# Kernel tuning notes

Measured on AMD Instinct MI355X. Metric: run time of the kernel, lower is better.

## Reference

```python
import jax, jax.numpy as jnp
import numpy as np

EPS = 1e-5
NUM_GROUPS = 32


def setup_inputs() -> dict:
    key = jax.random.key(0)
    ks = jax.random.split(key, 4)
    B, C, H, W = 8, 128, 64, 64
    x = jax.random.normal(ks[0], (B, C, H, W), dtype=jnp.float32)
    gamma = jnp.ones((C,), dtype=jnp.float32)
    beta = jnp.zeros((C,), dtype=jnp.float32)
    # 1x1 convs stored as dense [out, in] matrices (kaiming-ish scale)
    w_qkv = jax.random.normal(ks[1], (3 * C, C), dtype=jnp.float32) * (1.0 / np.sqrt(C))
    b_qkv = jnp.zeros((3 * C,), dtype=jnp.float32)
    w_out = jax.random.normal(ks[2], (C, C), dtype=jnp.float32) * (1.0 / np.sqrt(C))
    b_out = jnp.zeros((C,), dtype=jnp.float32)
    return {"x": x, "gamma": gamma, "beta": beta, "w_qkv": w_qkv,
            "b_qkv": b_qkv, "w_out": w_out, "b_out": b_out}


def _group_norm(x, gamma, beta):
    B, C, H, W = x.shape
    xg = x.reshape(B, NUM_GROUPS, C // NUM_GROUPS, H, W)
    mean = jnp.mean(xg, axis=(2, 3, 4), keepdims=True)
    var = jnp.var(xg, axis=(2, 3, 4), keepdims=True)
    xn = ((xg - mean) * jax.lax.rsqrt(var + EPS)).reshape(B, C, H, W)
    return xn * gamma[None, :, None, None] + beta[None, :, None, None]


def reference(x, gamma, beta, w_qkv, b_qkv, w_out, b_out):
    B, C, H, W = x.shape
    hw = H * W
    xn = _group_norm(x, gamma, beta)
    # 1x1 conv C -> 3C
    qkv = jnp.einsum('oc,bchw->bohw', w_qkv, xn) + b_qkv[None, :, None, None]
    q, k, v = jnp.split(qkv, 3, axis=1)           # each [B, C, H, W]
    q = q.reshape(B, C, hw).transpose(0, 2, 1)    # [B, hw, C]
    k = k.reshape(B, C, hw)                       # [B, C, hw]
    v = v.reshape(B, C, hw).transpose(0, 2, 1)    # [B, hw, C]
    scale = C ** (-0.5)
    weights = jnp.einsum('bnc,bcm->bnm', q, k) * scale  # [B, hw, hw]
    attn = jax.nn.softmax(weights, axis=-1)
    out = jnp.einsum('bnm,bmc->bnc', attn, v)     # [B, hw, C]
    out = out.reshape(B, H, W, C).transpose(0, 3, 1, 2)  # [B, C, H, W]
    out = jnp.einsum('oc,bchw->bohw', w_out, out) + b_out[None, :, None, None]
    return out + x
```

## Files before the change

kernel.cpp:

```cpp
#include <hip/hip_runtime.h>

typedef __attribute__((ext_vector_type(8))) short short8;
typedef __attribute__((ext_vector_type(4))) float f32x4;
typedef unsigned short u16;
typedef unsigned int u32;

__device__ __forceinline__ float bf2f(u16 h) {
  union { u32 u; float f; } c; c.u = ((u32)h) << 16; return c.f;
}
__device__ __forceinline__ u16 f2bf(float f) {
  union { float f; u32 u; } c; c.f = f;
  u32 u = c.u;
  u32 r = u + 0x7fffu + ((u >> 16) & 1u);
  return (u16)(r >> 16);
}
__device__ __forceinline__ f32x4 mfma16(short8 a, short8 b, f32x4 c) {
  return __builtin_amdgcn_mfma_f32_16x16x32_bf16(a, b, c, 0, 0, 0);
}
__device__ __forceinline__ u32 cvtpk(float lo, float hi) {
  u32 r;
  asm("v_cvt_pk_bf16_f32 %0, %1, %2" : "=v"(r) : "v"(lo), "v"(hi));
  return r;
}
__device__ __forceinline__ void gl2lds(const u16* g, u16* l) {
  __builtin_amdgcn_global_load_lds(
      (const __attribute__((address_space(1))) void*)g,
      (__attribute__((address_space(3))) void*)l, 16, 0, 0);
}

#define WAIT_BAR(N) \
  asm volatile("s_waitcnt vmcnt(" #N ")\n\ts_barrier" ::: "memory")
#define MEM_FENCE() asm volatile("" ::: "memory")

__device__ __forceinline__ bool bf_mode(const void* gamma) {
  return ((const u16*)gamma)[0] == 0x3F80u;
}
__device__ __forceinline__ void load8(const void* p, size_t idx, bool isbf,
                                      float* o) {
  if (isbf) {
    const u16* q = (const u16*)p + idx;
    uint4 v = *(const uint4*)q;
    u32 w[4] = {v.x, v.y, v.z, v.w};
#pragma unroll
    for (int j = 0; j < 4; ++j) {
      o[2 * j]     = bf2f((u16)(w[j] & 0xffffu));
      o[2 * j + 1] = bf2f((u16)(w[j] >> 16));
    }
  } else {
    const float* q = (const float*)p + idx;
    float4 a = *(const float4*)q;
    float4 b = *(const float4*)(q + 4);
    o[0] = a.x; o[1] = a.y; o[2] = a.z; o[3] = a.w;
    o[4] = b.x; o[5] = b.y; o[6] = b.z; o[7] = b.w;
  }
}
__device__ __forceinline__ float ldf(const void* p, size_t i, bool isbf) {
  return isbf ? bf2f(((const u16*)p)[i]) : ((const float*)p)[i];
}

__global__ __launch_bounds__(256) void stats_kernel(
    const void* __restrict__ x, const void* __restrict__ gamma,
    const void* __restrict__ w_qkv, const void* __restrict__ w_out,
    u16* __restrict__ w_bf, float* __restrict__ stats) {
  bool isbf = bf_mode(gamma);
  int bg = blockIdx.x;
  if (!isbf) {
    int i = bg * 256 + threadIdx.x;
    float v = (i < 49152) ? ((const float*)w_qkv)[i]
                          : ((const float*)w_out)[i - 49152];
    w_bf[i] = f2bf(v);
  }
  int b = bg >> 5, g = bg & 31;
  size_t base = ((size_t)b * 128 + g * 4) << 12;
  float s = 0.f, ss = 0.f;
  for (int i = threadIdx.x; i < 2048; i += 256) {
    float v[8];
    load8(x, base + (size_t)i * 8, isbf, v);
#pragma unroll
    for (int j = 0; j < 8; ++j) { s += v[j]; ss += v[j] * v[j]; }
  }
#pragma unroll
  for (int off = 32; off; off >>= 1) {
    s += __shfl_xor(s, off);
    ss += __shfl_xor(ss, off);
  }
  __shared__ float red[8];
  int wv = threadIdx.x >> 6, lane = threadIdx.x & 63;
  if (lane == 0) { red[wv] = s; red[4 + wv] = ss; }
  __syncthreads();
  if (threadIdx.x == 0) {
    float st = red[0] + red[1] + red[2] + red[3];
    float sst = red[4] + red[5] + red[6] + red[7];
    float mean = st * (1.f / 16384.f);
    float var = sst * (1.f / 16384.f) - mean * mean;
    stats[bg * 2] = mean;
    stats[bg * 2 + 1] = rsqrtf(var + 1e-5f);
  }
}

__global__ __launch_bounds__(256) void qkv_fused_kernel(
    const void* __restrict__ x, const float* __restrict__ stats,
    const void* __restrict__ gamma, const void* __restrict__ beta,
    const void* __restrict__ w_qkv_in, const void* __restrict__ b_qkv,
    const u16* __restrict__ w_bf, u16* __restrict__ Qt,
    u16* __restrict__ Kt_bfm, u16* __restrict__ Kt_fpm,
    u16* __restrict__ V) {
  bool isbf = bf_mode(gamma);
  const u16* wq = isbf ? (const u16*)w_qkv_in : w_bf;
  u16* Kt = isbf ? Kt_bfm : Kt_fpm;
  int nt = blockIdx.x, b = blockIdx.y;
  int n0 = nt * 64;
  int t = threadIdx.x;
  __shared__ __align__(16) u16 shb[9216];
  u16* xn = shb;
  {
    int cg = t >> 3, ng = t & 7;
    float mean = stats[(b * 32 + cg) * 2];
    float rstd = stats[(b * 32 + cg) * 2 + 1];
    float vals[4][8];
#pragma unroll
    for (int cc = 0; cc < 4; ++cc) {
      int c = cg * 4 + cc;
      float sc = ldf(gamma, c, isbf) * rstd;
      float sh = ldf(beta, c, isbf) - mean * sc;
      float v[8];
      load8(x, (((size_t)b * 128 + c) << 12) + n0 + ng * 8, isbf, v);
#pragma unroll
      for (int j = 0; j < 8; ++j) vals[cc][j] = v[j] * sc + sh;
    }
#pragma unroll
    for (int j = 0; j < 8; ++j) {
      ushort4 o;
      o.x = f2bf(vals[0][j]);
      o.y = f2bf(vals[1][j]);
      o.z = f2bf(vals[2][j]);
      o.w = f2bf(vals[3][j]);
      *(ushort4*)(xn + (ng * 8 + j) * 136 + cg * 4) = o;
    }
  }
  __syncthreads();
  int wv = t >> 6, lane = t & 63, l15 = lane & 15, quad = lane >> 4;
  short8 bfr[4][4];
#pragma unroll
  for (int mt = 0; mt < 4; ++mt)
#pragma unroll
    for (int kk = 0; kk < 4; ++kk)
      bfr[mt][kk] = *(const short8*)(xn + (mt * 16 + l15) * 136 + kk * 32 + quad * 8);
  __syncthreads();

  u16* res = shb;
#pragma unroll
  for (int g = 0; g < 3; ++g) {
#pragma unroll
    for (int rd = 0; rd < 2; ++rd) {
      int tl = rd * 4 + wv;
      int otg = g * 8 + tl;
      short8 a[4];
#pragma unroll
      for (int kk = 0; kk < 4; ++kk)
        a[kk] = *(const short8*)(wq + (size_t)(otg * 16 + l15) * 128 + kk * 32 + quad * 8);
      int o0 = otg * 16 + quad * 4;
      float bias[4];
#pragma unroll
      for (int r = 0; r < 4; ++r) bias[r] = ldf(b_qkv, o0 + r, isbf);
      int c0 = tl * 16 + quad * 4;
#pragma unroll
      for (int mt = 0; mt < 4; ++mt) {
        f32x4 acc = (f32x4){0.f, 0.f, 0.f, 0.f};
#pragma unroll
        for (int kk = 0; kk < 4; ++kk) acc = mfma16(a[kk], bfr[mt][kk], acc);
        int nl = mt * 16 + l15;
        if (g < 2) {
          ushort4 o;
          o.x = f2bf(acc[0] + bias[0]);
          o.y = f2bf(acc[1] + bias[1]);
          o.z = f2bf(acc[2] + bias[2]);
          o.w = f2bf(acc[3] + bias[3]);
          *(ushort4*)(res + nl * 136 + c0) = o;
        } else {
#pragma unroll
          for (int r = 0; r < 4; ++r)
            res[(c0 + r) * 72 + nl] = f2bf(acc[r] + bias[r]);
        }
      }
    }
    __syncthreads();
    if (g < 2) {
      int n = t >> 2, seg = t & 3;
      const uint4* src = (const uint4*)(res + n * 136 + seg * 32);
      uint4* dst = (uint4*)((g == 0 ? Qt : Kt) +
                            ((size_t)b * 4096 + n0 + n) * 128 + seg * 32);
#pragma unroll
      for (int i = 0; i < 4; ++i) dst[i] = src[i];
    } else {
      int c = t >> 1, hf = t & 1;
      const uint4* src = (const uint4*)(res + c * 72 + hf * 32);
      uint4* dst = (uint4*)(V + ((size_t)b * 128 + c) * 4096 + n0 + hf * 32);
#pragma unroll
      for (int i = 0; i < 4; ++i) dst[i] = src[i];
    }
    __syncthreads();
  }
}

__global__ __launch_bounds__(512, 1) void flash_kernel(
    const u16* __restrict__ Qt, const u16* __restrict__ Kt_bfm,
    const u16* __restrict__ Kt_fpm, const u16* __restrict__ V,
    u16* __restrict__ attn, const void* __restrict__ gamma, int fuse,
    const void* __restrict__ w_out_in, const u16* __restrict__ w_bf_out,
    const void* __restrict__ b_out, const void* __restrict__ x,
    void* __restrict__ out) {
  bool isbf = bf_mode(gamma);
  const u16* Kt = isbf ? Kt_bfm : Kt_fpm;
  int b = blockIdx.x, qt = blockIdx.y;
  int t = threadIdx.x;
  int wv = t >> 6, lane = t & 63;
  int l15 = lane & 15, quad = lane >> 4;
  int rset = wv >> 1, h = wv & 1;
  __shared__ __align__(16) u16 smem[32768];
  u16* kb0 = smem;
  u16* vb0 = smem + 16384;
  const u16* Kb = Kt + (size_t)b * 4096 * 128;
  const u16* Vg = V + (size_t)b * 128 * 4096;

  auto issueK = [&](int tile, u16* dst) {
    int m = tile * 64;
#pragma unroll
    for (int i2 = 0; i2 < 2; ++i2) {
      int i = wv * 2 + i2;
      int Rp = i * 4 + (lane >> 4);
      int Rs = (Rp & 32) | ((Rp & 12) << 1) | ((Rp & 16) >> 2) | (Rp & 3);
      gl2lds(Kb + (size_t)(m + Rs) * 128 + (((lane & 15) ^ (Rp & 15)) << 3),
             dst + i * 512);
    }
  };
  auto issueV = [&](int tile, u16* dst) {
    int m = tile * 64;
#pragma unroll
    for (int i2 = 0; i2 < 2; ++i2) {
      int i = wv * 2 + i2;
      int c = i * 8 + (lane >> 3);
      gl2lds(Vg + (size_t)c * 4096 + m + (((lane & 7) ^ (c & 7)) << 3),
             dst + i * 512);
    }
  };

  int wq = qt * 128 + rset * 32;
  const float qs = 0.12753251f;
  const float M = 10.0f;
  short8 qf[2][4];
#pragma unroll
  for (int rs = 0; rs < 2; ++rs)
#pragma unroll
    for (int kk = 0; kk < 4; ++kk) {
      short8 raw = *(const short8*)(
          Qt + ((size_t)b * 4096 + wq + rs * 16 + l15) * 128 + kk * 32 + quad * 8);
      short8 o;
#pragma unroll
      for (int j = 0; j < 8; ++j) o[j] = (short)f2bf(bf2f((u16)raw[j]) * qs);
      qf[rs][kk] = o;
    }
  asm volatile("s_waitcnt vmcnt(0)" ::: "memory");

  issueK(0, kb0);
  MEM_FENCE();
  issueV(0, vb0);
  MEM_FENCE();
  issueK(1, kb0 + 8192);
  MEM_FENCE();

  float ls[2] = {0.f, 0.f};
  f32x4 acc[2][8];
#pragma unroll
  for (int rs = 0; rs < 2; ++rs)
#pragma unroll
    for (int ct = 0; ct < 8; ++ct) acc[rs][ct] = (f32x4){0.f, 0.f, 0.f, 0.f};

  for (int kt = 0; kt < 64; ++kt) {
    int s = kt & 1;
    u16* kbs = kb0 + s * 8192;
    u16* vbs = vb0 + s * 8192;
    if (kt < 63) { WAIT_BAR(4); } else { WAIT_BAR(2); }
    if (kt < 63) issueV(kt + 1, vb0 + (s ^ 1) * 8192);
    MEM_FENCE();
    f32x4 sacc[2][2];
#pragma unroll
    for (int rs = 0; rs < 2; ++rs)
#pragma unroll
      for (int mt = 0; mt < 2; ++mt) sacc[rs][mt] = (f32x4){0.f, 0.f, 0.f, 0.f};
    __builtin_amdgcn_s_setprio(1);
#pragma unroll
    for (int mt = 0; mt < 2; ++mt) {
      int R = h * 32 + mt * 16 + l15;
      short8 kf[4];
#pragma unroll
      for (int kk = 0; kk < 4; ++kk)
        kf[kk] = *(const short8*)(&kbs[R * 128 + (((kk * 4 + quad) ^ l15) << 3)]);
#pragma unroll
      for (int rs = 0; rs < 2; ++rs)
#pragma unroll
        for (int kk = 0; kk < 4; ++kk)
          sacc[rs][mt] = mfma16(kf[kk], qf[rs][kk], sacc[rs][mt]);
    }
    __builtin_amdgcn_s_setprio(0);
    short8 pa[2];
#pragma unroll
    for (int rs = 0; rs < 2; ++rs) {
      union { u32 w[4]; short8 s8; } pk;
#pragma unroll
      for (int mt = 0; mt < 2; ++mt)
#pragma unroll
        for (int pr = 0; pr < 2; ++pr) {
          float p0 = __builtin_amdgcn_exp2f(sacc[rs][mt][2 * pr] - M);
          float p1 = __builtin_amdgcn_exp2f(sacc[rs][mt][2 * pr + 1] - M);
          ls[rs] += p0 + p1;
          pk.w[mt * 2 + pr] = cvtpk(p0, p1);
        }
      pa[rs] = pk.s8;
    }
    if (kt < 63) { WAIT_BAR(4); } else { WAIT_BAR(0); }
    if (kt < 62) issueK(kt + 2, kbs);
    MEM_FENCE();
    __builtin_amdgcn_s_setprio(1);
#pragma unroll
    for (int ct = 0; ct < 8; ++ct) {
      int c = ct * 16 + l15;
      int ch = ((h * 4 + quad) ^ (c & 7)) & 7;
      short8 vbf = *(const short8*)(&vbs[c * 64 + ch * 8]);
      acc[0][ct] = mfma16(pa[0], vbf, acc[0][ct]);
      acc[1][ct] = mfma16(pa[1], vbf, acc[1][ct]);
    }
    __builtin_amdgcn_s_setprio(0);
  }
  __syncthreads();

  float lsum[2][4];
#pragma unroll
  for (int rs = 0; rs < 2; ++rs) {
    float v = ls[rs];
    v += __shfl_xor(v, 16);
    v += __shfl_xor(v, 32);
#pragma unroll
    for (int r = 0; r < 4; ++r)
      lsum[rs][r] = __shfl(v, quad * 20 + r);
  }

  if (!fuse) {
    float* ef = (float*)smem;
#pragma unroll
    for (int rs = 0; rs < 2; ++rs) {
      if (h) {
#pragma unroll
        for (int ct = 0; ct < 8; ++ct)
          *(f32x4*)&ef[((rset * 8 + ct) * 64 + lane) * 4] = acc[rs][ct];
        if (rs == 0) {
#pragma unroll
          for (int j = 0; j < 8; ++j)
            ef[8192 + (rset * 64 + lane) * 8 + j] = lsum[j >> 2][j & 3];
        }
      }
      __syncthreads();
      if (!h) {
#pragma unroll
        for (int ct = 0; ct < 8; ++ct) {
          f32x4 o = *(const f32x4*)&ef[((rset * 8 + ct) * 64 + lane) * 4];
          acc[rs][ct] += o;
        }
        if (rs == 0) {
#pragma unroll
          for (int j = 0; j < 8; ++j)
            lsum[j >> 2][j & 3] += ef[8192 + (rset * 64 + lane) * 8 + j];
        }
      }
      __syncthreads();
    }
    if (!h) {
#pragma unroll
      for (int rs = 0; rs < 2; ++rs)
#pragma unroll
        for (int r = 0; r < 4; ++r) lsum[rs][r] = 1.f / lsum[rs][r];
#pragma unroll
      for (int rs = 0; rs < 2; ++rs)
#pragma unroll
        for (int ct = 0; ct < 8; ++ct)
#pragma unroll
          for (int r = 0; r < 4; ++r) {
            int n = wq + rs * 16 + quad * 4 + r;
            attn[((size_t)b * 4096 + n) * 128 + ct * 16 + l15] =
                f2bf(acc[rs][ct][r] * lsum[rs][r]);
          }
    }
    return;
  }

  const u16* wo = isbf ? (const u16*)w_out_in : w_bf_out;
  int o_row = wv * 16;
  int o0 = o_row + quad * 4;
  int nbase = qt * 128;
  float xres[8][4];
#pragma unroll
  for (int nt16 = 0; nt16 < 8; ++nt16)
#pragma unroll
    for (int r = 0; r < 4; ++r) {
      size_t idx = ((size_t)b * 128 + o0 + r) * 4096 + nbase + nt16 * 16 + l15;
      xres[nt16][r] = ldf(x, idx, isbf);
    }
  short8 wa[4];
#pragma unroll
  for (int kk = 0; kk < 4; ++kk)
    wa[kk] = *(const short8*)(wo + (size_t)(o_row + l15) * 128 + kk * 32 + quad * 8);

  u16* Otile = smem;
  float* mrg = (float*)(smem + 17408);
  float* lmr = (float*)(smem + 25600);
  if (h) {
#pragma unroll
    for (int j = 0; j < 8; ++j)
      lmr[(rset * 64 + lane) * 8 + j] = lsum[j >> 2][j & 3];
  }
  __syncthreads();
  if (!h) {
#pragma unroll
    for (int rs = 0; rs < 2; ++rs)
#pragma unroll
      for (int r = 0; r < 4; ++r)
        lsum[rs][r] =
            1.f / (lsum[rs][r] + lmr[(rset * 64 + lane) * 8 + rs * 4 + r]);
  }
  __syncthreads();
#pragma unroll
  for (int rs = 0; rs < 2; ++rs)
#pragma unroll
    for (int cg2 = 0; cg2 < 2; ++cg2) {
      if (h) {
#pragma unroll
        for (int c4 = 0; c4 < 4; ++c4)
          *(f32x4*)&mrg[((rset * 4 + c4) * 64 + lane) * 4] = acc[rs][cg2 * 4 + c4];
      }
      __syncthreads();
      if (!h) {
#pragma unroll
        for (int c4 = 0; c4 < 4; ++c4) {
          int ct = cg2 * 4 + c4;
          f32x4 o = *(const f32x4*)&mrg[((rset * 4 + c4) * 64 + lane) * 4];
          int nloc = rset * 32 + rs * 16 + quad * 4;
#pragma unroll
          for (int r = 0; r < 4; ++r)
            Otile[(nloc + r) * 136 + ct * 16 + l15] =
                f2bf((acc[rs][ct][r] + o[r]) * lsum[rs][r]);
        }
      }
      __syncthreads();
    }
  f32x4 acc2[8];
#pragma unroll
  for (int nt16 = 0; nt16 < 8; ++nt16) {
    acc2[nt16] = (f32x4){0.f, 0.f, 0.f, 0.f};
#pragma unroll
    for (int kk = 0; kk < 4; ++kk) {
      short8 bfrag = *(const short8*)(
          &Otile[(nt16 * 16 + l15) * 136 + kk * 32 + quad * 8]);
      acc2[nt16] = mfma16(wa[kk], bfrag, acc2[nt16]);
    }
  }
  float bias[4];
#pragma unroll
  for (int r = 0; r < 4; ++r) bias[r] = ldf(b_out, o0 + r, isbf);
#pragma unroll
  for (int nt16 = 0; nt16 < 8; ++nt16) {
#pragma unroll
    for (int r = 0; r < 4; ++r) {
      size_t idx = ((size_t)b * 128 + o0 + r) * 4096 + nbase + nt16 * 16 + l15;
      float val = acc2[nt16][r] + bias[r] + xres[nt16][r];
      if (isbf) ((u16*)out)[idx] = f2bf(val);
      else      ((float*)out)[idx] = val;
    }
  }
}

__global__ __launch_bounds__(256) void proj_kernel(
    const u16* __restrict__ attn, const void* __restrict__ w_out_in,
    const u16* __restrict__ w_bf_out, const void* __restrict__ b_out,
    const void* __restrict__ x, const void* __restrict__ gamma,
    void* __restrict__ out) {
  bool isbf = bf_mode(gamma);
  const u16* wo = isbf ? (const u16*)w_out_in : w_bf_out;
  int nt = blockIdx.x, ot = blockIdx.y, b = blockIdx.z;
  int wv = threadIdx.x >> 6, lane = threadIdx.x & 63;
  int l15 = lane & 15, quad = lane >> 4;
  int o_row = ot * 64 + wv * 16;
  short8 a[4];
#pragma unroll
  for (int kk = 0; kk < 4; ++kk)
    a[kk] = *(const short8*)(wo + (size_t)(o_row + l15) * 128 + kk * 32 + quad * 8);
  const u16* bbase = attn + ((size_t)b * 4096 + nt * 64) * 128;
  f32x4 acc[4];
#pragma unroll
  for (int mt = 0; mt < 4; ++mt) {
    acc[mt] = (f32x4){0.f, 0.f, 0.f, 0.f};
#pragma unroll
    for (int kk = 0; kk < 4; ++kk) {
      short8 bf = *(const short8*)(bbase + (size_t)(mt * 16 + l15) * 128 + kk * 32 + quad * 8);
      acc[mt] = mfma16(a[kk], bf, acc[mt]);
    }
  }
  int o0 = o_row + quad * 4;
  float bias[4];
#pragma unroll
  for (int r = 0; r < 4; ++r) bias[r] = ldf(b_out, o0 + r, isbf);
#pragma unroll
  for (int mt = 0; mt < 4; ++mt) {
    int n = nt * 64 + mt * 16 + l15;
#pragma unroll
    for (int r = 0; r < 4; ++r) {
      size_t idx = ((size_t)b * 128 + o0 + r) * 4096 + n;
      float val = acc[mt][r] + bias[r] + ldf(x, idx, isbf);
      if (isbf) ((u16*)out)[idx] = f2bf(val);
      else      ((float*)out)[idx] = val;
    }
  }
}

__global__ __launch_bounds__(256) void copy_kernel(
    const void* __restrict__ x, const void* __restrict__ gamma,
    void* __restrict__ out, int n) {
  bool isbf = bf_mode(gamma);
  int i = blockIdx.x * 256 + threadIdx.x;
  if (i < n) {
    if (isbf) ((u16*)out)[i] = ((const u16*)x)[i];
    else      ((float*)out)[i] = ((const float*)x)[i];
  }
}

extern "C" void kernel_launch(void* const* d_in, const int* in_sizes, int n_in,
                              void* d_out, int out_size, void* d_ws, size_t ws_size,
                              hipStream_t stream) {
  (void)in_sizes; (void)n_in;
  const void* x     = d_in[0];
  const void* gamma = d_in[1];
  const void* beta  = d_in[2];
  const void* w_qkv = d_in[3];
  const void* b_qkv = d_in[4];
  const void* w_out = d_in[5];
  const void* b_out = d_in[6];
  char* ws = (char*)d_ws;

  const size_t MB = 1u << 20;
  const size_t need = 16 * MB + 4096;
  if (ws_size < need) {
    copy_kernel<<<dim3((out_size + 255) / 256), dim3(256), 0, stream>>>(
        x, gamma, d_out, out_size);
    return;
  }
  int fuse = (ws_size >= 24 * MB + 262144) ? 1 : 0;
  u16 *Qt, *Kt_bfm, *Kt_fpm, *Vb, *w_bf, *attn;
  float* stats;
  if (fuse) {
    Qt     = (u16*)ws;
    Kt_bfm = (u16*)(ws + 8 * MB);
    Kt_fpm = Kt_bfm;
    Vb     = (u16*)(ws + 16 * MB);
    stats  = (float*)(ws + 24 * MB);
    w_bf   = (u16*)(ws + 24 * MB + 4096);
    attn   = Qt;
  } else {
    Qt     = (u16*)ws;
    Kt_bfm = (u16*)(ws + 8 * MB);
    w_bf   = (u16*)(ws + 8 * MB + 4096);
    stats  = (float*)(ws + 16 * MB);
    Vb     = (u16*)d_out;
    Kt_fpm = (u16*)d_out + 4194304;
    attn   = Qt;
  }

  stats_kernel<<<dim3(256), dim3(256), 0, stream>>>(
      x, gamma, w_qkv, w_out, w_bf, stats);
  qkv_fused_kernel<<<dim3(64, 8), dim3(256), 0, stream>>>(
      x, stats, gamma, beta, w_qkv, b_qkv, w_bf, Qt, Kt_bfm, Kt_fpm, Vb);
  flash_kernel<<<dim3(8, 32), dim3(512), 0, stream>>>(
      Qt, Kt_bfm, Kt_fpm, Vb, attn, gamma, fuse,
      w_out, w_bf + 49152, b_out, x, d_out);
  if (!fuse)
    proj_kernel<<<dim3(64, 2, 8), dim3(256), 0, stream>>>(
        attn, w_out, w_bf + 49152, b_out, x, gamma, d_out);
}
```

Measured before the change: 178.7 us.

## Restructure flash K/V prefetch into single-barrier double buffer with precomputed pointers

Replaces the staggered K/V prefetch schedule (K two tiles ahead, V one tile ahead, two waits and barriers per iteration) with a simpler double buffer. It issues K and V for the next tile together after a single full wait and barrier. Global source pointers are computed once and advanced by a fixed stride instead of recomputing the swizzled addresses each time. The loop is unrolled by two so the buffer index is a constant. This removes one barrier per iteration and some address arithmetic, but the prefetch distance for K drops from two tiles to one and each wait drains all outstanding loads, which may expose more memory latency.

```diff
diff --git a/kernel.cpp b/kernel.cpp
--- a/kernel.cpp
+++ b/kernel.cpp
@@ -218,32 +218,21 @@
   int l15 = lane & 15, quad = lane >> 4;
   int rset = wv >> 1, h = wv & 1;
   __shared__ __align__(16) u16 smem[32768];
-  u16* kb0 = smem;
-  u16* vb0 = smem + 16384;
   const u16* Kb = Kt + (size_t)b * 4096 * 128;
   const u16* Vg = V + (size_t)b * 128 * 4096;
 
-  auto issueK = [&](int tile, u16* dst) {
-    int m = tile * 64;
-#pragma unroll
-    for (int i2 = 0; i2 < 2; ++i2) {
-      int i = wv * 2 + i2;
-      int Rp = i * 4 + (lane >> 4);
-      int Rs = (Rp & 32) | ((Rp & 12) << 1) | ((Rp & 16) >> 2) | (Rp & 3);
-      gl2lds(Kb + (size_t)(m + Rs) * 128 + (((lane & 15) ^ (Rp & 15)) << 3),
-             dst + i * 512);
-    }
-  };
-  auto issueV = [&](int tile, u16* dst) {
-    int m = tile * 64;
-#pragma unroll
-    for (int i2 = 0; i2 < 2; ++i2) {
-      int i = wv * 2 + i2;
-      int c = i * 8 + (lane >> 3);
-      gl2lds(Vg + (size_t)c * 4096 + m + (((lane & 7) ^ (c & 7)) << 3),
-             dst + i * 512);
-    }
-  };
+  const u16 *kp0, *kp1, *vp0, *vp1;
+  {
+    int i0 = wv * 2, i1 = wv * 2 + 1;
+    int Rp0 = i0 * 4 + (lane >> 4), Rp1 = i1 * 4 + (lane >> 4);
+    int Rs0 = (Rp0 & 32) | ((Rp0 & 12) << 1) | ((Rp0 & 16) >> 2) | (Rp0 & 3);
+    int Rs1 = (Rp1 & 32) | ((Rp1 & 12) << 1) | ((Rp1 & 16) >> 2) | (Rp1 & 3);
+    kp0 = Kb + (size_t)Rs0 * 128 + (((lane & 15) ^ (Rp0 & 15)) << 3);
+    kp1 = Kb + (size_t)Rs1 * 128 + (((lane & 15) ^ (Rp1 & 15)) << 3);
+    int c0 = i0 * 8 + (lane >> 3), c1 = i1 * 8 + (lane >> 3);
+    vp0 = Vg + (size_t)c0 * 4096 + (((lane & 7) ^ (c0 & 7)) << 3);
+    vp1 = Vg + (size_t)c1 * 4096 + (((lane & 7) ^ (c1 & 7)) << 3);
+  }
 
   int wq = qt * 128 + rset * 32;
   const float qs = 0.12753251f;
@@ -262,11 +251,15 @@
     }
   asm volatile("s_waitcnt vmcnt(0)" ::: "memory");
 
-  issueK(0, kb0);
-  MEM_FENCE();
-  issueV(0, vb0);
-  MEM_FENCE();
-  issueK(1, kb0 + 8192);
+  {
+    int i0 = wv * 2, i1 = wv * 2 + 1;
+    gl2lds(kp0, smem + i0 * 512);
+    gl2lds(kp1, smem + i1 * 512);
+    kp0 += 8192; kp1 += 8192;
+    gl2lds(vp0, smem + 16384 + i0 * 512);
+    gl2lds(vp1, smem + 16384 + i1 * 512);
+    vp0 += 64; vp1 += 64;
+  }
   MEM_FENCE();
 
   float ls[2] = {0.f, 0.f};
@@ -276,12 +269,21 @@
 #pragma unroll
     for (int ct = 0; ct < 8; ++ct) acc[rs][ct] = (f32x4){0.f, 0.f, 0.f, 0.f};
 
-  for (int kt = 0; kt < 64; ++kt) {
-    int s = kt & 1;
-    u16* kbs = kb0 + s * 8192;
-    u16* vbs = vb0 + s * 8192;
-    if (kt < 63) { WAIT_BAR(4); } else { WAIT_BAR(2); }
-    if (kt < 63) issueV(kt + 1, vb0 + (s ^ 1) * 8192);
+  auto body = [&](int s_, bool do_issue) __attribute__((always_inline)) {
+    u16* kbs = smem + s_ * 8192;
+    u16* vbs = smem + 16384 + s_ * 8192;
+    WAIT_BAR(0);
+    if (do_issue) {
+      int i0 = wv * 2, i1 = wv * 2 + 1;
+      u16* kd = smem + (s_ ^ 1) * 8192;
+      u16* vd = smem + 16384 + (s_ ^ 1) * 8192;
+      gl2lds(kp0, kd + i0 * 512);
+      gl2lds(kp1, kd + i1 * 512);
+      kp0 += 8192; kp1 += 8192;
+      gl2lds(vp0, vd + i0 * 512);
+      gl2lds(vp1, vd + i1 * 512);
+      vp0 += 64; vp1 += 64;
+    }
     MEM_FENCE();
     f32x4 sacc[2][2];
 #pragma unroll
@@ -318,9 +320,6 @@
         }
       pa[rs] = pk.s8;
     }
-    if (kt < 63) { WAIT_BAR(4); } else { WAIT_BAR(0); }
-    if (kt < 62) issueK(kt + 2, kbs);
-    MEM_FENCE();
     __builtin_amdgcn_s_setprio(1);
 #pragma unroll
     for (int ct = 0; ct < 8; ++ct) {
@@ -331,6 +330,11 @@
       acc[1][ct] = mfma16(pa[1], vbf, acc[1][ct]);
     }
     __builtin_amdgcn_s_setprio(0);
+  };
+
+  for (int kp = 0; kp < 32; ++kp) {
+    body(0, true);
+    body(1, kp < 31);
   }
   __syncthreads();
 
```

Result: faster. 173.2 us (-3.1%).
